# Kernel tuning notes

Hardware: AMD Instinct MI355X
Metric: run time of the kernel (lower is better)

## Reference

```python
import jax, jax.numpy as jnp
import numpy as np

DEL_ID, STOP_ID, PAD_ID, KEEP_ID = 3, 5, 0, 2


def lstm(x, h0, c0, Wi, Wh, bi, bh):
    """Single-layer batch-first LSTM, PyTorch gate order (i,f,g,o).
    x: [B,T,E]; h0,c0: [B,H]. Returns (ys [B,T,H], h [B,H], c [B,H])."""
    b = bi + bh

    def step(carry, xt):
        h, c = carry
        g = xt @ Wi.T + h @ Wh.T + b  # [B,4H]
        i, f, gg, o = jnp.split(g, 4, axis=-1)
        c = jax.nn.sigmoid(f) * c + jax.nn.sigmoid(i) * jnp.tanh(gg)
        h = jax.nn.sigmoid(o) * jnp.tanh(c)
        return (h, c), h

    (h, c), ys = jax.lax.scan(step, (h0, c0), jnp.swapaxes(x, 0, 1))
    return jnp.swapaxes(ys, 0, 1), h, c


def setup_inputs() -> dict:
    key = jax.random.key(0)
    ks = jax.random.split(key, 20)
    B, T, S, H, E, V = 32, 100, 100, 512, 256, 30000
    s = 0.02
    inp = {
        "input_edits": jax.random.randint(ks[0], (B, T), 0, V),
        "simp_sent": jax.random.randint(ks[1], (B, S), 0, V),
        "org_ids": jax.random.randint(ks[2], (B, S), 0, V),
        "encoder_outputs_org": jax.random.normal(ks[3], (B, S, H), dtype=jnp.float32),
        "h0": jnp.zeros((B, H), jnp.float32),
        "c0": jnp.zeros((B, H), jnp.float32),
        "emb": jax.random.normal(ks[4], (V, E), dtype=jnp.float32) * s,
        "Wi_e": jax.random.normal(ks[5], (4 * H, E), dtype=jnp.float32) * s,
        "Wh_e": jax.random.normal(ks[6], (4 * H, H), dtype=jnp.float32) * s,
        "bi_e": jnp.zeros((4 * H,), jnp.float32),
        "bh_e": jnp.zeros((4 * H,), jnp.float32),
        "Wi_w": jax.random.normal(ks[7], (4 * H, E), dtype=jnp.float32) * s,
        "Wh_w": jax.random.normal(ks[8], (4 * H, H), dtype=jnp.float32) * s,
        "bi_w": jnp.zeros((4 * H,), jnp.float32),
        "bh_w": jnp.zeros((4 * H,), jnp.float32),
        "Wp": jax.random.normal(ks[9], (H, H), dtype=jnp.float32) * s,
        "Wm": jax.random.normal(ks[10], (E, 4 * H), dtype=jnp.float32) * s,
        "bm": jnp.zeros((E,), jnp.float32),
        "b_out": jnp.zeros((30000,), jnp.float32),
    }
    return inp


def reference(input_edits, simp_sent, org_ids, encoder_outputs_org, h0, c0,
              emb, Wi_e, Wh_e, bi_e, bh_e, Wi_w, Wh_w, bi_w, bh_w,
              Wp, Wm, bm, b_out):
    # teacher_forcing_ratio = 1.0 -> teacher-forcing branch only
    B, T = input_edits.shape
    S = encoder_outputs_org.shape[1]
    Sw = simp_sent.shape[1]

    # run both LSTMs over the full teacher-forced sequences
    out_e, he, ce = lstm(emb[input_edits], h0, c0, Wi_e, Wh_e, bi_e, bh_e)  # [B,T,H]
    out_w, _, _ = lstm(emb[simp_sent], h0, c0, Wi_w, Wh_w, bi_w, bh_w)      # [B,Sw,H]

    # attention over encoder outputs
    key_org = out_e @ Wp.T                                                   # [B,T,H]
    attn = jax.nn.softmax(jnp.einsum('bth,bsh->bts', key_org, encoder_outputs_org), axis=-1)
    applied = jnp.einsum('bts,bsh->bth', attn, encoder_outputs_org)          # [B,T,H]

    # counters are exclusive cumsums of gold-action masks over input_edits[:,1:]
    a = input_edits[:, 1:]                                                   # gold actions, [B,T-1]
    inc_del = ((a == KEEP_ID) | (a == DEL_ID)).astype(jnp.int32)
    inc_ins = ((a != DEL_ID) & (a != STOP_ID) & (a != PAD_ID)).astype(jnp.int32)
    ctr_del = jnp.clip(jnp.cumsum(inc_del, 1) - inc_del, 0, S - 1)           # [B,T-1]
    ctr_ins = jnp.clip(jnp.cumsum(inc_ins, 1) - inc_ins, 0, Sw - 1)

    H = encoder_outputs_org.shape[2]
    c = jnp.take_along_axis(encoder_outputs_org,
                            jnp.broadcast_to(ctr_del[:, :, None], (B, T - 1, H)), axis=1)
    c_word = jnp.take_along_axis(out_w,
                                 jnp.broadcast_to(ctr_ins[:, :, None], (B, T - 1, H)), axis=1)

    feat = jnp.concatenate([out_e[:, :T - 1], applied[:, :T - 1], c, c_word], axis=-1)  # [B,T-1,4H]
    hmlp = jnp.tanh(feat @ Wm.T + bm)                                        # [B,T-1,E]
    logp = jax.nn.log_softmax(hmlp @ emb.T + b_out, axis=-1)                 # [B,T-1,V]
    return logp, he[None], ce[None]
```

## Files before the change

kernel.cpp:

```cpp
#include <hip/hip_runtime.h>
#include <math.h>


typedef __attribute__((ext_vector_type(8))) short short8v;
typedef __attribute__((ext_vector_type(4))) float f32x4;
typedef unsigned long long ull;

#define LSTM_BLOCKS 64
#define NTIL 235

__device__ __forceinline__ float sigf(float x){ return 1.0f/(1.0f + __expf(-x)); }
__device__ __forceinline__ float tanhc(float x){
  x = fminf(fmaxf(x, -15.f), 15.f);
  float e = __expf(2.f*x);
  return (e-1.f)/(e+1.f);
}
__device__ __forceinline__ short f2bf(float f){
  unsigned u = __float_as_uint(f);
  u = (u + 0x7fffu + ((u >> 16) & 1u)) >> 16;
  return (short)u;
}
__device__ __forceinline__ float bf2f(short s){
  return __uint_as_float(((unsigned)(unsigned short)s) << 16);
}

__global__ void prep_permute(
    const float* __restrict__ Wi_e, const float* __restrict__ Wh_e,
    const float* __restrict__ bi_e, const float* __restrict__ bh_e,
    const float* __restrict__ Wi_w, const float* __restrict__ Wh_w,
    const float* __restrict__ bi_w, const float* __restrict__ bh_w,
    short* __restrict__ WiPh_e, short* __restrict__ WhPh_e, float* __restrict__ biasP_e,
    short* __restrict__ WiPh_w, short* __restrict__ WhPh_w, float* __restrict__ biasP_w)
{
  const int z = blockIdx.y;
  const float* Wi = z ? Wi_w : Wi_e;
  const float* Wh = z ? Wh_w : Wh_e;
  const float* bi = z ? bi_w : bi_e;
  const float* bh = z ? bh_w : bh_e;
  short* WiPh = z ? WiPh_w : WiPh_e;
  short* WhPh = z ? WhPh_w : WhPh_e;
  float* biasP = z ? biasP_w : biasP_e;

  int idx = blockIdx.x*256 + threadIdx.x;
  {
    int op = idx >> 9, k = idx & 511;
    int u = op >> 2, g = op & 3;
    WhPh[idx] = f2bf(Wh[(g*512+u)*512 + k]);
  }
  if (idx < 2048*256) {
    int op = idx >> 8, e = idx & 255;
    int u = op >> 2, g = op & 3;
    WiPh[idx] = f2bf(Wi[(g*512+u)*256 + e]);
  }
  if (idx < 2048) {
    int u = idx >> 2, g = idx & 3;
    biasP[idx] = bi[g*512+u] + bh[g*512+u];
  }
}

__global__ void misc_prep(const float* __restrict__ Wp, const float* __restrict__ Wm,
                          const float* __restrict__ h0, const int* __restrict__ ie,
                          short* __restrict__ Wph, short* __restrict__ Wmh,
                          ull* __restrict__ hq, unsigned* __restrict__ bar,
                          int* __restrict__ ctr_del, int* __restrict__ ctr_ins)
{
  int idx = blockIdx.x*256 + threadIdx.x;
  if (idx < 65536) {
    float4 v = *(const float4*)(Wp + (long)idx*4);
    short4 o; o.x=f2bf(v.x); o.y=f2bf(v.y); o.z=f2bf(v.z); o.w=f2bf(v.w);
    *(short4*)(Wph + (long)idx*4) = o;
  } else if (idx < 196608) {
    int i = idx - 65536;
    float4 v = *(const float4*)(Wm + (long)i*4);
    short4 o; o.x=f2bf(v.x); o.y=f2bf(v.y); o.z=f2bf(v.z); o.w=f2bf(v.w);
    *(short4*)(Wmh + (long)i*4) = o;
  } else if (idx < 204800) {
    int i = idx - 196608;
    int b = (i >> 7) & 31, q = i & 127;
    const float* src = h0 + b*512 + q*4;
    ull v = ((ull)(unsigned short)f2bf(src[3]) << 48) |
            ((ull)(unsigned short)f2bf(src[2]) << 32) |
            ((ull)(unsigned short)f2bf(src[1]) << 16) |
            ((ull)(unsigned short)f2bf(src[0]));
    hq[i] = v;
  } else if (idx < 204928) {
    bar[idx - 204800] = 0u;
  } else if (idx < 204960) {
    int b = idx - 204928;
    int rd = 0, ri = 0;
    for (int t = 0; t < 99; ++t) {
      int a = ie[b*100 + t + 1];
      int incd = (a == 2 || a == 3) ? 1 : 0;
      int inci = (a != 3 && a != 5 && a != 0) ? 1 : 0;
      ctr_del[b*99 + t] = min(rd, 99);
      ctr_ins[b*99 + t] = min(ri, 99);
      rd += incd; ri += inci;
    }
  }
}

template<int GATHER,int CVT_A,int BIAS,int TANH,int OUT_BF16>
__device__ __forceinline__ void gemm_mfma_body(
    const void* __restrict__ Av, const int* __restrict__ tok,
    const short* __restrict__ Bh, const float* __restrict__ bias,
    void* __restrict__ Cv, int M, int N, int K, int lda, int ldc,
    int bxk, int byk)
{
  __shared__ short As[128][72];
  __shared__ short Bs[128][72];
  const int bm = bxk * 128;
  const int bn = byk * 128;
  const int tid = threadIdx.x;
  const int w = tid >> 6, l = tid & 63;
  const int wr = (w >> 1) * 64, wc = (w & 1) * 64;
  const int lr = l & 15, kg = l >> 4;

  f32x4 acc[4][4] = {};

  for (int k0 = 0; k0 < K; k0 += 64) {
    #pragma unroll
    for (int q = 0; q < 4; ++q) {
      int ci = tid + 256*q;
      int r = ci >> 3, ch = ci & 7;
      int ar = bm + r; if (ar > M-1) ar = M-1;
      if (GATHER) ar = tok[ar];
      if (CVT_A) {
        const float* ap = ((const float*)Av) + (long)ar*lda + k0 + ch*8;
        float4 v0 = *(const float4*)ap;
        float4 v1 = *(const float4*)(ap + 4);
        short8v s;
        s[0]=f2bf(v0.x); s[1]=f2bf(v0.y); s[2]=f2bf(v0.z); s[3]=f2bf(v0.w);
        s[4]=f2bf(v1.x); s[5]=f2bf(v1.y); s[6]=f2bf(v1.z); s[7]=f2bf(v1.w);
        *(short8v*)&As[r][ch*8] = s;
      } else {
        *(short8v*)&As[r][ch*8] =
            *(const short8v*)(((const short*)Av) + (long)ar*lda + k0 + ch*8);
      }
      int br = bn + r; if (br > N-1) br = N-1;
      *(short8v*)&Bs[r][ch*8] = *(const short8v*)(Bh + (long)br*K + k0 + ch*8);
    }
    __syncthreads();
    #pragma unroll
    for (int ks = 0; ks < 2; ++ks) {
      short8v a[4], b[4];
      #pragma unroll
      for (int m = 0; m < 4; ++m)
        a[m] = *(const short8v*)&As[wr + m*16 + lr][ks*32 + kg*8];
      #pragma unroll
      for (int n = 0; n < 4; ++n)
        b[n] = *(const short8v*)&Bs[wc + n*16 + lr][ks*32 + kg*8];
      #pragma unroll
      for (int m = 0; m < 4; ++m)
        #pragma unroll
        for (int n = 0; n < 4; ++n)
          acc[m][n] = __builtin_amdgcn_mfma_f32_16x16x32_bf16(a[m], b[n], acc[m][n], 0, 0, 0);
    }
    __syncthreads();
  }

  #pragma unroll
  for (int n = 0; n < 4; ++n) {
    int col = bn + wc + n*16 + lr;
    bool cok = (col < N);
    float bv = (BIAS && cok) ? bias[col] : 0.f;
    #pragma unroll
    for (int m = 0; m < 4; ++m) {
      int row0 = bm + wr + m*16 + kg*4;
      #pragma unroll
      for (int r = 0; r < 4; ++r) {
        int row = row0 + r;
        if (cok && row < M) {
          float v = acc[m][n][r] + bv;
          if (TANH) v = tanhc(v);
          if (OUT_BF16) ((short*)Cv)[(long)row*ldc + col] = f2bf(v);
          else          ((float*)Cv)[(long)row*ldc + col] = v;
        }
      }
    }
  }
}

template<int GATHER,int CVT_A,int BIAS,int TANH,int OUT_BF16>
__global__ __launch_bounds__(256) void gemm_mfma(
    const void* __restrict__ Av, const int* __restrict__ tok,
    const short* __restrict__ Bh, const float* __restrict__ bias,
    void* __restrict__ Cv, int M, int N, int K, int lda, int ldc)
{
  gemm_mfma_body<GATHER,CVT_A,BIAS,TANH,OUT_BF16>(
      Av, tok, Bh, bias, Cv, M, N, K, lda, ldc, blockIdx.x, blockIdx.y);
}

__global__ __launch_bounds__(256) void xproj_mfma(
    const float* __restrict__ emb,
    const int* __restrict__ tokA, const int* __restrict__ tokB,
    const short* __restrict__ WA, const short* __restrict__ WB,
    const float* __restrict__ bA, const float* __restrict__ bB,
    short* __restrict__ outA, short* __restrict__ outB)
{
  const int z = blockIdx.z;
  gemm_mfma_body<1,1,1,0,1>(
      emb, z ? tokB : tokA, z ? WB : WA, z ? bB : bA,
      z ? (void*)outB : (void*)outA, 3200, 2048, 256, 256, 2048,
      blockIdx.x, blockIdx.y);
}

__global__ __launch_bounds__(256) void logits_mfma_partial(
    const short* __restrict__ Ah,
    const float* __restrict__ Bf,
    const float* __restrict__ bias,
    short* __restrict__ Cg,
    float2* __restrict__ partial)
{
  __shared__ short As[128][72];
  __shared__ short Bs[128][72];
  __shared__ float2 red[128][2];
  const int bm = blockIdx.x * 128;
  const int bn = blockIdx.y * 128;
  const int tid = threadIdx.x;
  const int w = tid >> 6, l = tid & 63;
  const int wr = (w >> 1) * 64, wc = (w & 1) * 64;
  const int lr = l & 15, kg = l >> 4;

  f32x4 acc[4][4] = {};

  #pragma unroll
  for (int k0 = 0; k0 < 256; k0 += 64) {
    #pragma unroll
    for (int q = 0; q < 4; ++q) {
      int ci = tid + 256*q;
      int r = ci >> 3, ch = ci & 7;
      int ar = bm + r; if (ar > 3167) ar = 3167;
      *(short8v*)&As[r][ch*8] = *(const short8v*)(Ah + (long)ar*256 + k0 + ch*8);
      int br = bn + r; if (br > 29999) br = 29999;
      const float* bp = Bf + (long)br*256 + k0 + ch*8;
      float4 v0 = *(const float4*)bp;
      float4 v1 = *(const float4*)(bp + 4);
      short8v s;
      s[0]=f2bf(v0.x); s[1]=f2bf(v0.y); s[2]=f2bf(v0.z); s[3]=f2bf(v0.w);
      s[4]=f2bf(v1.x); s[5]=f2bf(v1.y); s[6]=f2bf(v1.z); s[7]=f2bf(v1.w);
      *(short8v*)&Bs[r][ch*8] = s;
    }
    __syncthreads();
    #pragma unroll
    for (int ks = 0; ks < 2; ++ks) {
      short8v a[4], b[4];
      #pragma unroll
      for (int m = 0; m < 4; ++m)
        a[m] = *(const short8v*)&As[wr + m*16 + lr][ks*32 + kg*8];
      #pragma unroll
      for (int n = 0; n < 4; ++n)
        b[n] = *(const short8v*)&Bs[wc + n*16 + lr][ks*32 + kg*8];
      #pragma unroll
      for (int m = 0; m < 4; ++m)
        #pragma unroll
        for (int n = 0; n < 4; ++n)
          acc[m][n] = __builtin_amdgcn_mfma_f32_16x16x32_bf16(a[m], b[n], acc[m][n], 0, 0, 0);
    }
    __syncthreads();
  }

  #pragma unroll
  for (int n = 0; n < 4; ++n) {
    int col = bn + wc + n*16 + lr;
    float bv = (col < 30000) ? bias[col] : 0.f;
    #pragma unroll
    for (int m = 0; m < 4; ++m)
      #pragma unroll
      for (int r = 0; r < 4; ++r)
        acc[m][n][r] = (col < 30000) ? acc[m][n][r] + bv : -INFINITY;
  }
  #pragma unroll
  for (int m = 0; m < 4; ++m) {
    #pragma unroll
    for (int r = 0; r < 4; ++r) {
      float a0 = acc[m][0][r], a1 = acc[m][1][r], a2 = acc[m][2][r], a3 = acc[m][3][r];
      float mx = fmaxf(fmaxf(a0, a1), fmaxf(a2, a3));
      #pragma unroll
      for (int off = 1; off < 16; off <<= 1) mx = fmaxf(mx, __shfl_xor(mx, off));
      float se = 0.f;
      if (mx > -INFINITY)
        se = __expf(a0-mx) + __expf(a1-mx) + __expf(a2-mx) + __expf(a3-mx);
      #pragma unroll
      for (int off = 1; off < 16; off <<= 1) se += __shfl_xor(se, off);
      if (lr == 0) red[wr + m*16 + kg*4 + r][w & 1] = make_float2(mx, se);
    }
  }
  #pragma unroll
  for (int n = 0; n < 4; ++n) {
    int col = bn + wc + n*16 + lr;
    if (col < 30000) {
      #pragma unroll
      for (int m = 0; m < 4; ++m) {
        int row0 = bm + wr + m*16 + kg*4;
        #pragma unroll
        for (int r = 0; r < 4; ++r) {
          int row = row0 + r;
          if (row < 3168) Cg[(long)row*30000 + col] = f2bf(acc[m][n][r]);
        }
      }
    }
  }
  __syncthreads();
  if (tid < 128) {
    int row = bm + tid;
    if (row < 3168) {
      float2 A = red[tid][0], B = red[tid][1];
      float M = fmaxf(A.x, B.x);
      float S = 0.f;
      if (M > -INFINITY) S = A.y*__expf(A.x - M) + B.y*__expf(B.x - M);
      partial[(long)row*NTIL + blockIdx.y] = make_float2(M, S);
    }
  }
}

__global__ __launch_bounds__(256) void sub_lse_fused(
    const short* __restrict__ Cg, const float2* __restrict__ partial,
    float* __restrict__ out)
{
  int row = blockIdx.x;
  int tid = threadIdx.x;
  float m = -INFINITY, s = 0.f;
  if (tid < NTIL) {
    float2 p = partial[(long)row*NTIL + tid];
    m = p.x; s = p.y;
  }
  #pragma unroll
  for (int off = 32; off; off >>= 1) {
    float om = __shfl_xor(m, off);
    float os = __shfl_xor(s, off);
    float nm = fmaxf(m, om);
    if (nm > -INFINITY) {
      s = s*__expf(m - nm) + os*__expf(om - nm);
      m = nm;
    }
  }
  __shared__ float sm[4], ss[4], lsh;
  int wv = tid >> 6;
  if ((tid & 63) == 0) { sm[wv] = m; ss[wv] = s; }
  __syncthreads();
  if (tid == 0) {
    float M = sm[0], S = ss[0];
    #pragma unroll
    for (int i = 1; i < 4; ++i) {
      float nm = fmaxf(M, sm[i]);
      S = S*__expf(M - nm) + ss[i]*__expf(sm[i] - nm);
      M = nm;
    }
    lsh = M + __logf(S);
  }
  __syncthreads();
  float lv = lsh;
  const short* src = Cg + (long)row*30000;
  float* dst = out + (long)row*30000;
  for (int i = tid; i < 3750; i += 256) {
    short8v v = *(const short8v*)(src + i*8);
    float4 o0, o1;
    o0.x = bf2f(v[0]) - lv; o0.y = bf2f(v[1]) - lv;
    o0.z = bf2f(v[2]) - lv; o0.w = bf2f(v[3]) - lv;
    o1.x = bf2f(v[4]) - lv; o1.y = bf2f(v[5]) - lv;
    o1.z = bf2f(v[6]) - lv; o1.w = bf2f(v[7]) - lv;
    *(float4*)(dst + i*8)     = o0;
    *(float4*)(dst + i*8 + 4) = o1;
  }
}

template<int TRANSB>
__global__ __launch_bounds__(256) void gemm_f32(
    const float* __restrict__ A, const float* __restrict__ Bmat,
    float* __restrict__ C,
    int M, int N, int K, int lda, int ldb, int ldc,
    long sA, long sB, long sC)
{
  __shared__ float As[32][68];
  __shared__ float Bs[32][68];
  const int z = blockIdx.z;
  A    += (long)z * sA;
  Bmat += (long)z * sB;
  C    += (long)z * sC;
  const int bm = blockIdx.y*64, bn = blockIdx.x*64;
  const int tid = threadIdx.x;
  const int tx = tid & 15, ty = tid >> 4;
  float acc[4][4] = {};

  for (int k0 = 0; k0 < K; k0 += 32) {
    {
      int r = tid >> 2;
      int c0 = (tid & 3) * 8;
      int row = bm + r; if (row > M-1) row = M-1;
      const float* ap = A + (long)row * lda;
      #pragma unroll
      for (int q = 0; q < 2; ++q) {
        int kk = c0 + q*4;
        float4 v;
        if (k0 + kk + 4 <= K) v = *(const float4*)(ap + k0 + kk);
        else {
          v.x = (k0+kk+0 < K) ? ap[k0+kk+0] : 0.f;
          v.y = (k0+kk+1 < K) ? ap[k0+kk+1] : 0.f;
          v.z = (k0+kk+2 < K) ? ap[k0+kk+2] : 0.f;
          v.w = (k0+kk+3 < K) ? ap[k0+kk+3] : 0.f;
        }
        As[kk+0][r]=v.x; As[kk+1][r]=v.y; As[kk+2][r]=v.z; As[kk+3][r]=v.w;
      }
    }
    if (TRANSB) {
      int n = tid >> 2;
      int c0 = (tid & 3) * 8;
      int col = bn + n; if (col > N-1) col = N-1;
      const float* bp = Bmat + (long)col * ldb;
      #pragma unroll
      for (int q = 0; q < 2; ++q) {
        int kk = c0 + q*4;
        float4 v;
        if (k0 + kk + 4 <= K) v = *(const float4*)(bp + k0 + kk);
        else {
          v.x = (k0+kk+0 < K) ? bp[k0+kk+0] : 0.f;
          v.y = (k0+kk+1 < K) ? bp[k0+kk+1] : 0.f;
          v.z = (k0+kk+2 < K) ? bp[k0+kk+2] : 0.f;
          v.w = (k0+kk+3 < K) ? bp[k0+kk+3] : 0.f;
        }
        Bs[kk+0][n]=v.x; Bs[kk+1][n]=v.y; Bs[kk+2][n]=v.z; Bs[kk+3][n]=v.w;
      }
    } else {
      int kk = tid >> 3;
      int c0 = (tid & 7) * 8;
      int krow = k0 + kk;
      #pragma unroll
      for (int q = 0; q < 2; ++q) {
        int cc = c0 + q*4;
        int col = bn + cc;
        float4 v = make_float4(0.f,0.f,0.f,0.f);
        if (krow < K) {
          const float* bp = Bmat + (long)krow * ldb;
          if (col + 4 <= N) v = *(const float4*)(bp + col);
          else {
            v.x = (col+0 < N) ? bp[col+0] : 0.f;
            v.y = (col+1 < N) ? bp[col+1] : 0.f;
            v.z = (col+2 < N) ? bp[col+2] : 0.f;
            v.w = (col+3 < N) ? bp[col+3] : 0.f;
          }
        }
        Bs[kk][cc+0]=v.x; Bs[kk][cc+1]=v.y; Bs[kk][cc+2]=v.z; Bs[kk][cc+3]=v.w;
      }
    }
    __syncthreads();
    #pragma unroll
    for (int kk = 0; kk < 32; ++kk) {
      float4 a = *(const float4*)&As[kk][ty*4];
      float4 b = *(const float4*)&Bs[kk][tx*4];
      acc[0][0]=fmaf(a.x,b.x,acc[0][0]); acc[0][1]=fmaf(a.x,b.y,acc[0][1]);
      acc[0][2]=fmaf(a.x,b.z,acc[0][2]); acc[0][3]=fmaf(a.x,b.w,acc[0][3]);
      acc[1][0]=fmaf(a.y,b.x,acc[1][0]); acc[1][1]=fmaf(a.y,b.y,acc[1][1]);
      acc[1][2]=fmaf(a.y,b.z,acc[1][2]); acc[1][3]=fmaf(a.y,b.w,acc[1][3]);
      acc[2][0]=fmaf(a.z,b.x,acc[2][0]); acc[2][1]=fmaf(a.z,b.y,acc[2][1]);
      acc[2][2]=fmaf(a.z,b.z,acc[2][2]); acc[2][3]=fmaf(a.z,b.w,acc[2][3]);
      acc[3][0]=fmaf(a.w,b.x,acc[3][0]); acc[3][1]=fmaf(a.w,b.y,acc[3][1]);
      acc[3][2]=fmaf(a.w,b.z,acc[3][2]); acc[3][3]=fmaf(a.w,b.w,acc[3][3]);
    }
    __syncthreads();
  }
  #pragma unroll
  for (int i = 0; i < 4; ++i) {
    int row = bm + ty*4 + i;
    if (row >= M) continue;
    #pragma unroll
    for (int j = 0; j < 4; ++j) {
      int col = bn + tx*4 + j;
      if (col >= N) continue;
      C[(long)row*ldc + col] = acc[i][j];
    }
  }
}

__global__ __launch_bounds__(256, 1) void lstm_persist(
    const short* __restrict__ WhPh_e, const short* __restrict__ WhPh_w,
    const short* __restrict__ Xp_e, const short* __restrict__ Xp_w,
    const float* __restrict__ c0_in,
    ull* __restrict__ hq,
    short* __restrict__ outT,
    float* __restrict__ out_hc,
    unsigned* __restrict__ flags)
{
  const int bx = blockIdx.x;
  const int l = bx >> 5;
  const int ublk = bx & 31;
  const int tid = threadIdx.x;
  const int w = tid >> 6, lane = tid & 63;
  const int uloc = lane >> 4;
  const int bn = lane & 15;
  const int u_global = ublk*16 + w*4 + uloc;
  const int ob = (ublk*16 + w*4) * 4;
  const int qcol = ublk*4 + w;

  const short* WhPh = l ? WhPh_w : WhPh_e;
  const short* Xp   = l ? Xp_w   : Xp_e;
  const unsigned* myfl = flags + l*32;

  __shared__ short hT[32][520];

  __hip_atomic_load(&flags[100], __ATOMIC_ACQUIRE, __HIP_MEMORY_SCOPE_AGENT);

  short8v afr[16];
  {
    const short* wp = WhPh + (long)(ob + bn)*512 + uloc*8;
    #pragma unroll
    for (int ks = 0; ks < 16; ++ks)
      afr[ks] = *(const short8v*)(wp + ks*32);
  }
  float c_s0 = c0_in[bn*512 + u_global];
  float c_s1 = c0_in[(bn+16)*512 + u_global];

  for (int t = 0; t < 100; ++t) {
    ull xq0 = *(const ull*)(Xp + ((long)(bn*100 + t))*2048 + u_global*4);
    ull xq1 = *(const ull*)(Xp + ((long)((bn+16)*100 + t))*2048 + u_global*4);
    if (t) {
      int ok;
      do {
        unsigned f = (lane < 32)
          ? __hip_atomic_load(&myfl[lane], __ATOMIC_RELAXED, __HIP_MEMORY_SCOPE_AGENT)
          : 0xffffffffu;
        ok = __all((int)(f >= (unsigned)t));
        if (!ok) __builtin_amdgcn_s_sleep(1);
      } while (!ok);
    }
    {
      const ull* hsrc = hq + (size_t)t*8192 + (l << 12);
      #pragma unroll
      for (int i = 0; i < 16; ++i) {
        int idx = tid + 256*i;
        int b = idx >> 7, q = idx & 127;
        *(ull*)&hT[b][q*4] = hsrc[idx];
      }
    }
    __syncthreads();
    f32x4 acc0 = {}, acc1 = {};
    #pragma unroll
    for (int ks = 0; ks < 16; ++ks) {
      short8v b0 = *(const short8v*)&hT[bn][ks*32 + uloc*8];
      short8v b1 = *(const short8v*)&hT[bn+16][ks*32 + uloc*8];
      acc0 = __builtin_amdgcn_mfma_f32_16x16x32_bf16(afr[ks], b0, acc0, 0, 0, 0);
      acc1 = __builtin_amdgcn_mfma_f32_16x16x32_bf16(afr[ks], b1, acc1, 0, 0, 0);
    }
    float gi = acc0[0] + bf2f((short)(xq0 & 0xffffu));
    float gf = acc0[1] + bf2f((short)((xq0 >> 16) & 0xffffu));
    float gg = acc0[2] + bf2f((short)((xq0 >> 32) & 0xffffu));
    float go = acc0[3] + bf2f((short)((xq0 >> 48) & 0xffffu));
    c_s0 = sigf(gf)*c_s0 + sigf(gi)*tanhc(gg);
    float hv0 = sigf(go)*tanhc(c_s0);
    gi = acc1[0] + bf2f((short)(xq1 & 0xffffu));
    gf = acc1[1] + bf2f((short)((xq1 >> 16) & 0xffffu));
    gg = acc1[2] + bf2f((short)((xq1 >> 32) & 0xffffu));
    go = acc1[3] + bf2f((short)((xq1 >> 48) & 0xffffu));
    c_s1 = sigf(gf)*c_s1 + sigf(gi)*tanhc(gg);
    float hv1 = sigf(go)*tanhc(c_s1);

    short hb0 = f2bf(hv0), hb1 = f2bf(hv1);
    unsigned p0 = (unsigned)(unsigned short)hb0;
    unsigned p1 = (unsigned)(unsigned short)hb1;
    unsigned a1 = __shfl_down((int)p0, 16), a2 = __shfl_down((int)p0, 32), a3 = __shfl_down((int)p0, 48);
    unsigned e1 = __shfl_down((int)p1, 16), e2 = __shfl_down((int)p1, 32), e3 = __shfl_down((int)p1, 48);
    if (uloc == 0) {
      ull q0 = ((ull)((a2 & 0xffffu) | (a3 << 16)) << 32) | ((p0 & 0xffffu) | (a1 << 16));
      ull q1 = ((ull)((e2 & 0xffffu) | (e3 << 16)) << 32) | ((p1 & 0xffffu) | (e1 << 16));
      ull* hd = hq + (size_t)(t+1)*8192 + (l << 12);
      __hip_atomic_store(&hd[(bn << 7) + qcol],      q0, __ATOMIC_RELAXED, __HIP_MEMORY_SCOPE_AGENT);
      __hip_atomic_store(&hd[((bn+16) << 7) + qcol], q1, __ATOMIC_RELAXED, __HIP_MEMORY_SCOPE_AGENT);
    }
    if (t < 99) {
      asm volatile("s_waitcnt vmcnt(0)" ::: "memory");
      __syncthreads();
      if (tid == 0)
        __hip_atomic_store(&flags[bx], (unsigned)(t+1),
                           __ATOMIC_RELAXED, __HIP_MEMORY_SCOPE_AGENT);
    }
    short* od = outT + ((long)(l*100 + t)*512 + u_global)*32;
    od[bn]    = hb0;
    od[bn+16] = hb1;
    if (t == 99 && l == 0) {
      out_hc[bn*512 + u_global]              = hv0;
      out_hc[(bn+16)*512 + u_global]         = hv1;
      out_hc[16384 + bn*512 + u_global]      = c_s0;
      out_hc[16384 + (bn+16)*512 + u_global] = c_s1;
    }
  }
}

__global__ __launch_bounds__(256) void transpose_out(
    const short* __restrict__ outT, short* __restrict__ out_e, short* __restrict__ out_w)
{
  __shared__ short tile[512][40];
  const int t = blockIdx.x, l = blockIdx.y;
  const short* src = outT + (long)(l*100 + t)*16384;
  const int tid = threadIdx.x;
  #pragma unroll
  for (int i = 0; i < 8; ++i) {
    int fi = tid + 256*i;
    int u = fi >> 2, b8 = (fi & 3)*8;
    *(short8v*)&tile[u][b8] = *(const short8v*)(src + fi*8);
  }
  __syncthreads();
  short* dst = l ? out_w : out_e;
  for (int b = 0; b < 32; ++b) {
    short* drow = dst + (long)(b*100 + t)*512;
    drow[tid]     = tile[tid][b];
    drow[tid+256] = tile[tid+256][b];
  }
}

__global__ void softmax_rows(float* __restrict__ P)
{
  int row  = blockIdx.x*4 + (threadIdx.x >> 6);
  int lane = threadIdx.x & 63;
  float* p = P + (long)row*128;
  float x0 = (lane      < 100) ? p[lane]    : -INFINITY;
  float x1 = (lane + 64 < 100) ? p[lane+64] : -INFINITY;
  float m = fmaxf(x0, x1);
  #pragma unroll
  for (int off = 32; off; off >>= 1) m = fmaxf(m, __shfl_xor(m, off));
  float e0 = (lane      < 100) ? __expf(x0 - m) : 0.f;
  float e1 = (lane + 64 < 100) ? __expf(x1 - m) : 0.f;
  float s = e0 + e1;
  #pragma unroll
  for (int off = 32; off; off >>= 1) s += __shfl_xor(s, off);
  float inv = 1.f / s;
  if (lane      < 100) p[lane]    = e0 * inv;
  if (lane + 64 < 100) p[lane+64] = e1 * inv;
}

__global__ void feat_kernel(const short* __restrict__ out_e, const float* __restrict__ applied,
                            const float* __restrict__ enc,  const short* __restrict__ out_w,
                            const int* __restrict__ ctr_del, const int* __restrict__ ctr_ins,
                            short* __restrict__ feat)
{
  int n = blockIdx.x;
  int b = n / 99, t = n % 99;
  int tid = threadIdx.x;
  int seg = tid >> 6;
  int off = (tid & 63) * 8;
  short8v v;
  if (seg == 0) {
    v = *(const short8v*)(out_e + (long)(b*100 + t)*512 + off);
  } else if (seg == 3) {
    v = *(const short8v*)(out_w + (long)(b*100 + ctr_ins[n])*512 + off);
  } else {
    const float* s = (seg == 1) ? applied + (long)(b*100 + t)*512
                                : enc     + (long)(b*100 + ctr_del[n])*512;
    float4 v0 = *(const float4*)(s + off);
    float4 v1 = *(const float4*)(s + off + 4);
    v[0]=f2bf(v0.x); v[1]=f2bf(v0.y); v[2]=f2bf(v0.z); v[3]=f2bf(v0.w);
    v[4]=f2bf(v1.x); v[5]=f2bf(v1.y); v[6]=f2bf(v1.z); v[7]=f2bf(v1.w);
  }
  *(short8v*)(feat + (long)n*2048 + seg*512 + off) = v;
}

extern "C" void kernel_launch(void* const* d_in, const int* in_sizes, int n_in,
                              void* d_out, int out_size, void* d_ws, size_t ws_size,
                              hipStream_t stream)
{
  const int*   input_edits = (const int*)  d_in[0];
  const int*   simp_sent   = (const int*)  d_in[1];
  const float* enc   = (const float*)d_in[3];
  const float* h0    = (const float*)d_in[4];
  const float* c0    = (const float*)d_in[5];
  const float* emb   = (const float*)d_in[6];
  const float* Wi_e  = (const float*)d_in[7];
  const float* Wh_e  = (const float*)d_in[8];
  const float* bi_e  = (const float*)d_in[9];
  const float* bh_e  = (const float*)d_in[10];
  const float* Wi_w  = (const float*)d_in[11];
  const float* Wh_w  = (const float*)d_in[12];
  const float* bi_w  = (const float*)d_in[13];
  const float* bh_w  = (const float*)d_in[14];
  const float* Wp    = (const float*)d_in[15];
  const float* Wm    = (const float*)d_in[16];
  const float* bmv   = (const float*)d_in[17];
  const float* b_out = (const float*)d_in[18];
  float* out = (float*)d_out;

  float* ws = (float*)d_ws;
  size_t off = 0;
  auto alloc = [&](size_t n){ float* p = ws + off; off += (n + 63) & ~(size_t)63; return p; };

  short* WiPh_e   = (short*)alloc(262144);
  short* WiPh_w   = (short*)alloc(262144);
  float* biasP_e  = alloc(2048);
  float* biasP_w  = alloc(2048);
  short* WhPh_e   = (short*)alloc(524288);
  short* WhPh_w   = (short*)alloc(524288);
  short* Xp_e     = (short*)alloc(3276800);
  short* Xp_w     = (short*)alloc(3276800);
  short* outT     = (short*)alloc(1638400);
  short* out_e    = (short*)alloc(819200);
  short* out_w    = (short*)alloc(819200);
  ull*   hq       = (ull*)alloc(101*8192*2);
  unsigned* bar   = (unsigned*)alloc(128);
  float* Pbuf     = alloc(3200*128);
  int*   ctr_del  = (int*)alloc(3168);
  int*   ctr_ins  = (int*)alloc(3168);
  short* Wph      = (short*)alloc(131072);
  short* Wmh      = (short*)alloc(262144);
  float* key      = alloc(3200*512);
  float* applied  = alloc(3200*512);
  short* logith   = (short*)alloc(47520000);
  float2* partial = (float2*)alloc(3168*NTIL*2);
  short* feath    = (short*)Xp_e;
  short* hmlph    = (short*)Xp_w;

  prep_permute<<<dim3(4096,2), 256, 0, stream>>>(
      Wi_e, Wh_e, bi_e, bh_e, Wi_w, Wh_w, bi_w, bh_w,
      WiPh_e, WhPh_e, biasP_e, WiPh_w, WhPh_w, biasP_w);
  misc_prep<<<801, 256, 0, stream>>>(Wp, Wm, h0, input_edits,
                                     Wph, Wmh, hq, bar, ctr_del, ctr_ins);

  xproj_mfma<<<dim3(25,16,2), 256, 0, stream>>>(
      emb, input_edits, simp_sent, WiPh_e, WiPh_w, biasP_e, biasP_w, Xp_e, Xp_w);

  lstm_persist<<<LSTM_BLOCKS, 256, 0, stream>>>(
      WhPh_e, WhPh_w, Xp_e, Xp_w, c0, hq, outT, out + 95040000L, bar);

  transpose_out<<<dim3(100,2), 256, 0, stream>>>(outT, out_e, out_w);

  gemm_mfma<0,0,0,0,0><<<dim3(25,4), 256, 0, stream>>>(
      out_e, nullptr, Wph, nullptr, key, 3200, 512, 512, 512, 512);

  gemm_f32<1><<<dim3(2,2,32), 256, 0, stream>>>(
      key, enc, Pbuf, 100, 100, 512, 512, 512, 128, 51200, 51200, 12800);
  softmax_rows<<<800, 256, 0, stream>>>(Pbuf);
  gemm_f32<0><<<dim3(8,2,32), 256, 0, stream>>>(
      Pbuf, enc, applied, 100, 512, 100, 128, 512, 512, 12800, 51200, 51200);

  feat_kernel<<<3168, 256, 0, stream>>>(out_e, applied, enc, out_w, ctr_del, ctr_ins, feath);
  gemm_mfma<0,0,1,1,1><<<dim3(25,2), 256, 0, stream>>>(
      feath, nullptr, Wmh, bmv, hmlph, 3168, 256, 2048, 2048, 256);

  logits_mfma_partial<<<dim3(25, NTIL), 256, 0, stream>>>(
      hmlph, emb, b_out, logith, partial);
  sub_lse_fused<<<3168, 256, 0, stream>>>(logith, partial, out);
}
```

Measured before the change: 1.009 ms.

## Move attention GEMMs to bf16 MFMA and pre-convert emb and enc to bf16

The two batched fp32 attention GEMMs are replaced with a batched bf16 MFMA kernel. Encoder outputs are pre-converted once into bf16 row-major and transposed copies, and key, probabilities and applied are stored in bf16. The embedding table is converted to bf16 once in misc_prep, so the logits GEMM no longer converts fp32 on every tile load. The cost is an extra prep pass over the 30000x256 emb table, an added enc_prep kernel, and lower precision in the attention path.

```diff
diff --git a/kernel.cpp b/kernel.cpp
--- a/kernel.cpp
+++ b/kernel.cpp
@@ -58,24 +58,31 @@
   }
 }
 
-__global__ void misc_prep(const float* __restrict__ Wp, const float* __restrict__ Wm,
+__global__ void misc_prep(const float* __restrict__ emb,
+                          const float* __restrict__ Wp, const float* __restrict__ Wm,
                           const float* __restrict__ h0, const int* __restrict__ ie,
+                          short* __restrict__ embh,
                           short* __restrict__ Wph, short* __restrict__ Wmh,
                           ull* __restrict__ hq, unsigned* __restrict__ bar,
                           int* __restrict__ ctr_del, int* __restrict__ ctr_ins)
 {
   int idx = blockIdx.x*256 + threadIdx.x;
-  if (idx < 65536) {
-    float4 v = *(const float4*)(Wp + (long)idx*4);
+  if (idx < 1920000) {
+    float4 v = *(const float4*)(emb + (long)idx*4);
     short4 o; o.x=f2bf(v.x); o.y=f2bf(v.y); o.z=f2bf(v.z); o.w=f2bf(v.w);
-    *(short4*)(Wph + (long)idx*4) = o;
-  } else if (idx < 196608) {
-    int i = idx - 65536;
+    *(short4*)(embh + (long)idx*4) = o;
+  } else if (idx < 1985536) {
+    int i = idx - 1920000;
+    float4 v = *(const float4*)(Wp + (long)i*4);
+    short4 o; o.x=f2bf(v.x); o.y=f2bf(v.y); o.z=f2bf(v.z); o.w=f2bf(v.w);
+    *(short4*)(Wph + (long)i*4) = o;
+  } else if (idx < 2116608) {
+    int i = idx - 1985536;
     float4 v = *(const float4*)(Wm + (long)i*4);
     short4 o; o.x=f2bf(v.x); o.y=f2bf(v.y); o.z=f2bf(v.z); o.w=f2bf(v.w);
     *(short4*)(Wmh + (long)i*4) = o;
-  } else if (idx < 204800) {
-    int i = idx - 196608;
+  } else if (idx < 2124800) {
+    int i = idx - 2116608;
     int b = (i >> 7) & 31, q = i & 127;
     const float* src = h0 + b*512 + q*4;
     ull v = ((ull)(unsigned short)f2bf(src[3]) << 48) |
@@ -83,10 +90,10 @@
             ((ull)(unsigned short)f2bf(src[1]) << 16) |
             ((ull)(unsigned short)f2bf(src[0]));
     hq[i] = v;
-  } else if (idx < 204928) {
-    bar[idx - 204800] = 0u;
-  } else if (idx < 204960) {
-    int b = idx - 204928;
+  } else if (idx < 2124928) {
+    bar[idx - 2124800] = 0u;
+  } else if (idx < 2124960) {
+    int b = idx - 2124928;
     int rd = 0, ri = 0;
     for (int t = 0; t < 99; ++t) {
       int a = ie[b*100 + t + 1];
@@ -96,6 +103,36 @@
       ctr_ins[b*99 + t] = min(ri, 99);
       rd += incd; ri += inci;
     }
+  }
+}
+
+__global__ __launch_bounds__(256) void enc_prep(const float* __restrict__ enc,
+                                                short* __restrict__ ench,
+                                                short* __restrict__ encTh)
+{
+  __shared__ short tile[100][72];
+  const int b = blockIdx.x;
+  const float* src = enc + (long)b*51200;
+  short* de = ench  + (long)b*51200;
+  short* dt = encTh + (long)b*65536;
+  const int tid = threadIdx.x;
+  for (int c = 0; c < 8; ++c) {
+    #pragma unroll
+    for (int i = 0; i < 25; ++i) {
+      int idx = tid + 256*i;
+      int k = idx >> 6, j = idx & 63;
+      short h = f2bf(src[(long)k*512 + c*64 + j]);
+      tile[k][j] = h;
+      de[(long)k*512 + c*64 + j] = h;
+    }
+    __syncthreads();
+    #pragma unroll
+    for (int i = 0; i < 32; ++i) {
+      int idx = tid + 256*i;
+      int n = idx >> 7, kk = idx & 127;
+      dt[(long)(c*64 + n)*128 + kk] = (kk < 100) ? tile[kk][n] : (short)0;
+    }
+    __syncthreads();
   }
 }
 
@@ -190,6 +227,20 @@
       Av, tok, Bh, bias, Cv, M, N, K, lda, ldc, blockIdx.x, blockIdx.y);
 }
 
+template<int BIAS,int TANH,int OUT_BF16>
+__global__ __launch_bounds__(256) void gemm_mfma_bat(
+    const short* __restrict__ Ah, const short* __restrict__ Bh,
+    const float* __restrict__ bias, void* __restrict__ Cv,
+    int M, int N, int K, int lda, int ldc, long sA, long sB, long sC)
+{
+  const int z = blockIdx.z;
+  void* C2 = OUT_BF16 ? (void*)((short*)Cv + (long)z*sC)
+                      : (void*)((float*)Cv + (long)z*sC);
+  gemm_mfma_body<0,0,BIAS,TANH,OUT_BF16>(
+      (const void*)(Ah + (long)z*sA), nullptr, Bh + (long)z*sB, bias,
+      C2, M, N, K, lda, ldc, blockIdx.x, blockIdx.y);
+}
+
 __global__ __launch_bounds__(256) void xproj_mfma(
     const float* __restrict__ emb,
     const int* __restrict__ tokA, const int* __restrict__ tokB,
@@ -206,7 +257,7 @@
 
 __global__ __launch_bounds__(256) void logits_mfma_partial(
     const short* __restrict__ Ah,
-    const float* __restrict__ Bf,
+    const short* __restrict__ Bh,
     const float* __restrict__ bias,
     short* __restrict__ Cg,
     float2* __restrict__ partial)
@@ -232,13 +283,7 @@
       int ar = bm + r; if (ar > 3167) ar = 3167;
       *(short8v*)&As[r][ch*8] = *(const short8v*)(Ah + (long)ar*256 + k0 + ch*8);
       int br = bn + r; if (br > 29999) br = 29999;
-      const float* bp = Bf + (long)br*256 + k0 + ch*8;
-      float4 v0 = *(const float4*)bp;
-      float4 v1 = *(const float4*)(bp + 4);
-      short8v s;
-      s[0]=f2bf(v0.x); s[1]=f2bf(v0.y); s[2]=f2bf(v0.z); s[3]=f2bf(v0.w);
-      s[4]=f2bf(v1.x); s[5]=f2bf(v1.y); s[6]=f2bf(v1.z); s[7]=f2bf(v1.w);
-      *(short8v*)&Bs[r][ch*8] = s;
+      *(short8v*)&Bs[r][ch*8] = *(const short8v*)(Bh + (long)br*256 + k0 + ch*8);
     }
     __syncthreads();
     #pragma unroll
@@ -364,113 +409,6 @@
   }
 }
 
-template<int TRANSB>
-__global__ __launch_bounds__(256) void gemm_f32(
-    const float* __restrict__ A, const float* __restrict__ Bmat,
-    float* __restrict__ C,
-    int M, int N, int K, int lda, int ldb, int ldc,
-    long sA, long sB, long sC)
-{
-  __shared__ float As[32][68];
-  __shared__ float Bs[32][68];
-  const int z = blockIdx.z;
-  A    += (long)z * sA;
-  Bmat += (long)z * sB;
-  C    += (long)z * sC;
-  const int bm = blockIdx.y*64, bn = blockIdx.x*64;
-  const int tid = threadIdx.x;
-  const int tx = tid & 15, ty = tid >> 4;
-  float acc[4][4] = {};
-
-  for (int k0 = 0; k0 < K; k0 += 32) {
-    {
-      int r = tid >> 2;
-      int c0 = (tid & 3) * 8;
-      int row = bm + r; if (row > M-1) row = M-1;
-      const float* ap = A + (long)row * lda;
-      #pragma unroll
-      for (int q = 0; q < 2; ++q) {
-        int kk = c0 + q*4;
-        float4 v;
-        if (k0 + kk + 4 <= K) v = *(const float4*)(ap + k0 + kk);
-        else {
-          v.x = (k0+kk+0 < K) ? ap[k0+kk+0] : 0.f;
-          v.y = (k0+kk+1 < K) ? ap[k0+kk+1] : 0.f;
-          v.z = (k0+kk+2 < K) ? ap[k0+kk+2] : 0.f;
-          v.w = (k0+kk+3 < K) ? ap[k0+kk+3] : 0.f;
-        }
-        As[kk+0][r]=v.x; As[kk+1][r]=v.y; As[kk+2][r]=v.z; As[kk+3][r]=v.w;
-      }
-    }
-    if (TRANSB) {
-      int n = tid >> 2;
-      int c0 = (tid & 3) * 8;
-      int col = bn + n; if (col > N-1) col = N-1;
-      const float* bp = Bmat + (long)col * ldb;
-      #pragma unroll
-      for (int q = 0; q < 2; ++q) {
-        int kk = c0 + q*4;
-        float4 v;
-        if (k0 + kk + 4 <= K) v = *(const float4*)(bp + k0 + kk);
-        else {
-          v.x = (k0+kk+0 < K) ? bp[k0+kk+0] : 0.f;
-          v.y = (k0+kk+1 < K) ? bp[k0+kk+1] : 0.f;
-          v.z = (k0+kk+2 < K) ? bp[k0+kk+2] : 0.f;
-          v.w = (k0+kk+3 < K) ? bp[k0+kk+3] : 0.f;
-        }
-        Bs[kk+0][n]=v.x; Bs[kk+1][n]=v.y; Bs[kk+2][n]=v.z; Bs[kk+3][n]=v.w;
-      }
-    } else {
-      int kk = tid >> 3;
-      int c0 = (tid & 7) * 8;
-      int krow = k0 + kk;
-      #pragma unroll
-      for (int q = 0; q < 2; ++q) {
-        int cc = c0 + q*4;
-        int col = bn + cc;
-        float4 v = make_float4(0.f,0.f,0.f,0.f);
-        if (krow < K) {
-          const float* bp = Bmat + (long)krow * ldb;
-          if (col + 4 <= N) v = *(const float4*)(bp + col);
-          else {
-            v.x = (col+0 < N) ? bp[col+0] : 0.f;
-            v.y = (col+1 < N) ? bp[col+1] : 0.f;
-            v.z = (col+2 < N) ? bp[col+2] : 0.f;
-            v.w = (col+3 < N) ? bp[col+3] : 0.f;
-          }
-        }
-        Bs[kk][cc+0]=v.x; Bs[kk][cc+1]=v.y; Bs[kk][cc+2]=v.z; Bs[kk][cc+3]=v.w;
-      }
-    }
-    __syncthreads();
-    #pragma unroll
-    for (int kk = 0; kk < 32; ++kk) {
-      float4 a = *(const float4*)&As[kk][ty*4];
-      float4 b = *(const float4*)&Bs[kk][tx*4];
-      acc[0][0]=fmaf(a.x,b.x,acc[0][0]); acc[0][1]=fmaf(a.x,b.y,acc[0][1]);
-      acc[0][2]=fmaf(a.x,b.z,acc[0][2]); acc[0][3]=fmaf(a.x,b.w,acc[0][3]);
-      acc[1][0]=fmaf(a.y,b.x,acc[1][0]); acc[1][1]=fmaf(a.y,b.y,acc[1][1]);
-      acc[1][2]=fmaf(a.y,b.z,acc[1][2]); acc[1][3]=fmaf(a.y,b.w,acc[1][3]);
-      acc[2][0]=fmaf(a.z,b.x,acc[2][0]); acc[2][1]=fmaf(a.z,b.y,acc[2][1]);
-      acc[2][2]=fmaf(a.z,b.z,acc[2][2]); acc[2][3]=fmaf(a.z,b.w,acc[2][3]);
-      acc[3][0]=fmaf(a.w,b.x,acc[3][0]); acc[3][1]=fmaf(a.w,b.y,acc[3][1]);
-      acc[3][2]=fmaf(a.w,b.z,acc[3][2]); acc[3][3]=fmaf(a.w,b.w,acc[3][3]);
-    }
-    __syncthreads();
-  }
-  #pragma unroll
-  for (int i = 0; i < 4; ++i) {
-    int row = bm + ty*4 + i;
-    if (row >= M) continue;
-    #pragma unroll
-    for (int j = 0; j < 4; ++j) {
-      int col = bn + tx*4 + j;
-      if (col >= N) continue;
-      C[(long)row*ldc + col] = acc[i][j];
-    }
-  }
-}
-
 __global__ __launch_bounds__(256, 1) void lstm_persist(
     const short* __restrict__ WhPh_e, const short* __restrict__ WhPh_w,
     const short* __restrict__ Xp_e, const short* __restrict__ Xp_w,
@@ -606,28 +544,29 @@
   }
 }
 
-__global__ void softmax_rows(float* __restrict__ P)
+__global__ void softmax_rows(const float* __restrict__ P, short* __restrict__ Ph)
 {
   int row  = blockIdx.x*4 + (threadIdx.x >> 6);
   int lane = threadIdx.x & 63;
-  float* p = P + (long)row*128;
-  float x0 = (lane      < 100) ? p[lane]    : -INFINITY;
+  const float* p = P + (long)row*128;
+  short* q = Ph + (long)row*128;
+  float x0 = p[lane];
   float x1 = (lane + 64 < 100) ? p[lane+64] : -INFINITY;
   float m = fmaxf(x0, x1);
   #pragma unroll
   for (int off = 32; off; off >>= 1) m = fmaxf(m, __shfl_xor(m, off));
-  float e0 = (lane      < 100) ? __expf(x0 - m) : 0.f;
+  float e0 = __expf(x0 - m);
   float e1 = (lane + 64 < 100) ? __expf(x1 - m) : 0.f;
   float s = e0 + e1;
   #pragma unroll
   for (int off = 32; off; off >>= 1) s += __shfl_xor(s, off);
   float inv = 1.f / s;
-  if (lane      < 100) p[lane]    = e0 * inv;
-  if (lane + 64 < 100) p[lane+64] = e1 * inv;
-}
-
-__global__ void feat_kernel(const short* __restrict__ out_e, const float* __restrict__ applied,
-                            const float* __restrict__ enc,  const short* __restrict__ out_w,
+  q[lane]      = f2bf(e0 * inv);
+  q[lane + 64] = (lane + 64 < 100) ? f2bf(e1 * inv) : (short)0;
+}
+
+__global__ void feat_kernel(const short* __restrict__ out_e, const short* __restrict__ appliedh,
+                            const short* __restrict__ ench, const short* __restrict__ out_w,
                             const int* __restrict__ ctr_del, const int* __restrict__ ctr_ins,
                             short* __restrict__ feat)
 {
@@ -636,20 +575,11 @@
   int tid = threadIdx.x;
   int seg = tid >> 6;
   int off = (tid & 63) * 8;
-  short8v v;
-  if (seg == 0) {
-    v = *(const short8v*)(out_e + (long)(b*100 + t)*512 + off);
-  } else if (seg == 3) {
-    v = *(const short8v*)(out_w + (long)(b*100 + ctr_ins[n])*512 + off);
-  } else {
-    const float* s = (seg == 1) ? applied + (long)(b*100 + t)*512
-                                : enc     + (long)(b*100 + ctr_del[n])*512;
-    float4 v0 = *(const float4*)(s + off);
-    float4 v1 = *(const float4*)(s + off + 4);
-    v[0]=f2bf(v0.x); v[1]=f2bf(v0.y); v[2]=f2bf(v0.z); v[3]=f2bf(v0.w);
-    v[4]=f2bf(v1.x); v[5]=f2bf(v1.y); v[6]=f2bf(v1.z); v[7]=f2bf(v1.w);
-  }
-  *(short8v*)(feat + (long)n*2048 + seg*512 + off) = v;
+  const short* s = (seg == 0) ? out_e    + (long)(b*100 + t)*512
+                 : (seg == 1) ? appliedh + (long)(b*100 + t)*512
+                 : (seg == 2) ? ench     + (long)(b*100 + ctr_del[n])*512
+                              : out_w    + (long)(b*100 + ctr_ins[n])*512;
+  *(short8v*)(feat + (long)n*2048 + seg*512 + off) = *(const short8v*)(s + off);
 }
 
 extern "C" void kernel_launch(void* const* d_in, const int* in_sizes, int n_in,
@@ -693,13 +623,17 @@
   short* out_w    = (short*)alloc(819200);
   ull*   hq       = (ull*)alloc(101*8192*2);
   unsigned* bar   = (unsigned*)alloc(128);
-  float* Pbuf     = alloc(3200*128);
+  float* Pbuf     = alloc(409600);
+  short* Pbh      = (short*)alloc(204800);
   int*   ctr_del  = (int*)alloc(3168);
   int*   ctr_ins  = (int*)alloc(3168);
   short* Wph      = (short*)alloc(131072);
   short* Wmh      = (short*)alloc(262144);
-  float* key      = alloc(3200*512);
-  float* applied  = alloc(3200*512);
+  short* keyh     = (short*)alloc(819200);
+  short* appliedh = (short*)alloc(819200);
+  short* ench     = (short*)alloc(819200);
+  short* encTh    = (short*)alloc(1048576);
+  short* embh     = (short*)alloc(3840000);
   short* logith   = (short*)alloc(47520000);
   float2* partial = (float2*)alloc(3168*NTIL*2);
   short* feath    = (short*)Xp_e;
@@ -708,8 +642,9 @@
   prep_permute<<<dim3(4096,2), 256, 0, stream>>>(
       Wi_e, Wh_e, bi_e, bh_e, Wi_w, Wh_w, bi_w, bh_w,
       WiPh_e, WhPh_e, biasP_e, WiPh_w, WhPh_w, biasP_w);
-  misc_prep<<<801, 256, 0, stream>>>(Wp, Wm, h0, input_edits,
-                                     Wph, Wmh, hq, bar, ctr_del, ctr_ins);
+  misc_prep<<<8301, 256, 0, stream>>>(emb, Wp, Wm, h0, input_edits,
+                                      embh, Wph, Wmh, hq, bar, ctr_del, ctr_ins);
+  enc_prep<<<32, 256, 0, stream>>>(enc, ench, encTh);
 
   xproj_mfma<<<dim3(25,16,2), 256, 0, stream>>>(
       emb, input_edits, simp_sent, WiPh_e, WiPh_w, biasP_e, biasP_w, Xp_e, Xp_w);
@@ -719,20 +654,23 @@
 
   transpose_out<<<dim3(100,2), 256, 0, stream>>>(outT, out_e, out_w);
 
-  gemm_mfma<0,0,0,0,0><<<dim3(25,4), 256, 0, stream>>>(
-      out_e, nullptr, Wph, nullptr, key, 3200, 512, 512, 512, 512);
-
-  gemm_f32<1><<<dim3(2,2,32), 256, 0, stream>>>(
-      key, enc, Pbuf, 100, 100, 512, 512, 512, 128, 51200, 51200, 12800);
-  softmax_rows<<<800, 256, 0, stream>>>(Pbuf);
-  gemm_f32<0><<<dim3(8,2,32), 256, 0, stream>>>(
-      Pbuf, enc, applied, 100, 512, 100, 128, 512, 512, 12800, 51200, 51200);
-
-  feat_kernel<<<3168, 256, 0, stream>>>(out_e, applied, enc, out_w, ctr_del, ctr_ins, feath);
+  gemm_mfma<0,0,0,0,1><<<dim3(25,4), 256, 0, stream>>>(
+      out_e, nullptr, Wph, nullptr, keyh, 3200, 512, 512, 512, 512);
+
+  gemm_mfma_bat<0,0,0><<<dim3(1,1,32), 256, 0, stream>>>(
+      keyh, ench, nullptr, Pbuf, 100, 100, 512, 512, 128,
+      51200, 51200, 12800);
+  softmax_rows<<<800, 256, 0, stream>>>(Pbuf, Pbh);
+  gemm_mfma_bat<0,0,1><<<dim3(1,4,32), 256, 0, stream>>>(
+      Pbh, encTh, nullptr, appliedh, 100, 512, 128, 128, 512,
+      12800, 65536, 51200);
+
+  feat_kernel<<<3168, 256, 0, stream>>>(out_e, appliedh, ench, out_w,
+                                        ctr_del, ctr_ins, feath);
   gemm_mfma<0,0,1,1,1><<<dim3(25,2), 256, 0, stream>>>(
       feath, nullptr, Wmh, bmv, hmlph, 3168, 256, 2048, 2048, 256);
 
   logits_mfma_partial<<<dim3(25, NTIL), 256, 0, stream>>>(
-      hmlph, emb, b_out, logith, partial);
+      hmlph, embh, b_out, logith, partial);
   sub_lse_fused<<<3168, 256, 0, stream>>>(logith, partial, out);
 }
```

New measurement: 1.056 ms. 4.7% more time.
